# Performance work log

Measured on AMD Instinct MI355X. Metric: run time of the kernel, lower is better.

## Reference

```python
import jax, jax.numpy as jnp
import numpy as np

B, H, W = 64, 512, 512
T = 100           # num_thresholds
R = 8             # defect regions per image (max label id)
BLOCK = 128       # defect regions are 128x128 blocks on a 4x4 grid
SAT = 1.0         # saturation_threshold (relative)


def setup_inputs() -> dict:
    key = jax.random.key(0)
    k1, _ = jax.random.split(key)
    preds = jax.random.uniform(k1, (B, H, W), dtype=jnp.float32)
    thresholds = jnp.linspace(0.0, 1.0, T).astype(jnp.float32)
    # Build a labeled GT mask: R disjoint 128x128 block regions per image,
    # labels 1..R (0 = background). This plays the role of measure.label(target).
    rng = np.random.default_rng(0)
    labels = np.zeros((B, H, W), dtype=np.int32)
    gb = H // BLOCK           # 4 blocks per side -> 16 candidate blocks
    nblocks = gb * gb
    for b in range(B):
        chosen = rng.permutation(nblocks)[:R]
        for rid, blk in enumerate(chosen, start=1):
            r, c = divmod(int(blk), gb)
            labels[b, r * BLOCK:(r + 1) * BLOCK, c * BLOCK:(c + 1) * BLOCK] = rid
    return {"preds": preds, "thresholds": thresholds, "labels": jnp.asarray(labels)}


def reference(preds, thresholds, labels):
    # preds: (B,H,W) float32 in [0,1); thresholds: (T,) sorted; labels: (B,H,W) int32, 0=bg.
    Bn, Hn, Wn = preds.shape
    Tn = thresholds.shape[0]
    flat_s = preds.reshape(-1)
    flat_l = labels.reshape(-1)
    # bucket[p] = number of thresholds <= score[p]; pixel passes thr[t] iff bucket > t.
    bucket = jnp.searchsorted(thresholds, flat_s, side='right')  # int in [0, T]
    # ---- background FP / TN per threshold (exact counts via histogram) ----
    bg = (flat_l == 0).astype(jnp.int32)
    bg_hist = jax.ops.segment_sum(bg, bucket, num_segments=Tn + 1)  # (T+1,)
    bg_total = bg_hist.sum()
    fp = (bg_total - jnp.cumsum(bg_hist)[:Tn]).astype(jnp.float32)  # fp[t] = #bg with score>=thr[t]
    tn = bg_total.astype(jnp.float32) - fp
    # ---- per-region TP per threshold (segmented histogram) ----
    bidx = jnp.repeat(jnp.arange(Bn), Hn * Wn)
    seg = bidx * R + (flat_l - 1)              # region id in [0, B*R)
    comb = seg * (Tn + 1) + bucket
    NSEG = Bn * R * (Tn + 1)
    comb = jnp.where(flat_l > 0, comb, NSEG)   # dump bg pixels in overflow slot
    hist = jax.ops.segment_sum(jnp.ones_like(bucket, dtype=jnp.int32), comb,
                               num_segments=NSEG + 1)[:NSEG].reshape(Bn, R, Tn + 1)
    area = hist.sum(-1)                                       # (B,R) defect areas
    tp = (area[..., None] - jnp.cumsum(hist, -1)[..., :Tn]).astype(jnp.float32)  # (B,R,T)
    sat = jnp.maximum(area.astype(jnp.float32) * SAT, 1.0)    # relative saturation
    valid = (area > 0).astype(jnp.float32)                    # guard empty regions
    spro = jnp.minimum(tp / sat[..., None], 1.0) * valid[..., None]
    spro_sum = spro.sum((0, 1))                               # (T,)
    n_def = jnp.maximum(valid.sum(), 1.0)
    mean_spro = spro_sum / n_def
    # ---- AUC over FPR (max_fpr = 1.0) ----
    denom = fp + tn
    fpr = jnp.where(denom > 0, fp / jnp.maximum(denom, 1.0), 0.0)
    order = jnp.argsort(fpr)
    x = fpr[order]
    y = mean_spro[order]
    auc = jnp.sum((x[1:] - x[:-1]) * (y[1:] + y[:-1]) * 0.5)  # trapezoid rule
    return auc
```

## Files before the change

### kernel.cpp

```cpp
#include <hip/hip_runtime.h>

#define B_N 64
#define H_N 512
#define W_N 512
#define T_N 100
#define TB  101
#define R_N 8
#define NLAB 9
#define BLOCKS_PER_IMG 16
#define PIX_PER_IMG (H_N * W_N)
#define PIX_PER_BLOCK (PIX_PER_IMG / BLOCKS_PER_IMG)

__global__ __launch_bounds__(256) void hist_kernel(
    const float* __restrict__ preds, const int* __restrict__ labels,
    const float* __restrict__ thr,
    int* __restrict__ region_hist,
    int* __restrict__ bg_hist)
{
    __shared__ float s_thr[T_N];
    __shared__ int whist[4][NLAB * TB];

    const int tid  = threadIdx.x;
    const int wave = tid >> 6;

    for (int i = tid; i < 4 * NLAB * TB; i += 256) ((int*)whist)[i] = 0;
    if (tid < T_N) s_thr[tid] = thr[tid];
    __syncthreads();

    const int img   = blockIdx.x / BLOCKS_PER_IMG;
    const int chunk = blockIdx.x % BLOCKS_PER_IMG;
    const long base = (long)img * PIX_PER_IMG + (long)chunk * PIX_PER_BLOCK;
    const float4* p4 = (const float4*)(preds + base);
    const int4*   l4 = (const int4*)(labels + base);
    int* __restrict__ myh = whist[wave];

    const int iters = PIX_PER_BLOCK / (256 * 4);
    for (int it = 0; it < iters; ++it) {
        float4 pv = p4[it * 256 + tid];
        int4   lv = l4[it * 256 + tid];
        float ps[4] = {pv.x, pv.y, pv.z, pv.w};
        int   ls[4] = {lv.x, lv.y, lv.z, lv.w};
#pragma unroll
        for (int j = 0; j < 4; ++j) {
            float s = ps[j];
            int k = (int)(s * (float)(T_N - 1)) + 1;
            k = max(0, min(T_N, k));
            while (k < T_N && s_thr[k] <= s) ++k;
            while (k > 0 && s_thr[k - 1] > s) --k;
            atomicAdd(&myh[ls[j] * TB + k], 1);
        }
    }
    __syncthreads();

    for (int i = tid; i < NLAB * TB; i += 256) {
        int v = whist[0][i] + whist[1][i] + whist[2][i] + whist[3][i];
        if (v) {
            int lab = i / TB;
            int t   = i - lab * TB;
            if (lab == 0)
                atomicAdd(&bg_hist[img * TB + t], v);
            else
                atomicAdd(&region_hist[(img * R_N + (lab - 1)) * TB + t], v);
        }
    }
}

__global__ __launch_bounds__(128) void region_kernel(
    const int* __restrict__ region_hist,
    float* __restrict__ spro_sum,
    int* __restrict__ n_def)
{
    __shared__ float spro_sh[R_N][T_N];
    __shared__ int validc[R_N];
    const int img = blockIdx.x;
    const int tid = threadIdx.x;

    if (tid < R_N) {
        const int* h = &region_hist[(img * R_N + tid) * TB];
        int area = 0;
        for (int t = 0; t < TB; ++t) area += h[t];
        float sat   = fmaxf((float)area, 1.0f);
        float valid = (area > 0) ? 1.0f : 0.0f;
        int csum = 0;
        for (int t = 0; t < T_N; ++t) {
            csum += h[t];
            float tp = (float)(area - csum);
            spro_sh[tid][t] = fminf(tp / sat, 1.0f) * valid;
        }
        validc[tid] = (area > 0) ? 1 : 0;
    }
    __syncthreads();

    if (tid < T_N) {
        float s = 0.0f;
        for (int r = 0; r < R_N; ++r) s += spro_sh[r][tid];
        atomicAdd(&spro_sum[tid], s);
    }
    if (tid == 0) {
        int v = 0;
        for (int r = 0; r < R_N; ++r) v += validc[r];
        atomicAdd(n_def, v);
    }
}

__global__ __launch_bounds__(128) void final_kernel(
    const int* __restrict__ bg_hist,
    const float* __restrict__ spro_sum,
    const int* __restrict__ n_def,
    float* __restrict__ out)
{
    __shared__ int    bgh[TB];
    __shared__ float  fpr_sh[T_N];
    __shared__ float  ms_sh[T_N];
    __shared__ int    order[T_N];
    __shared__ double contrib[T_N];
    const int tid = threadIdx.x;

    if (tid < TB) {
        int s = 0;
        for (int b = 0; b < B_N; ++b) s += bg_hist[b * TB + tid];
        bgh[tid] = s;
    }
    __syncthreads();

    if (tid < T_N) {
        int fp_i = 0;
        for (int k = tid + 1; k < TB; ++k) fp_i += bgh[k];
        int tot = fp_i;
        for (int k = 0; k <= tid; ++k) tot += bgh[k];
        float bgt = (float)tot;
        float fp  = (float)fp_i;
        fpr_sh[tid] = (bgt > 0.0f) ? fp / fmaxf(bgt, 1.0f) : 0.0f;
        float nd = fmaxf((float)(*n_def), 1.0f);
        ms_sh[tid] = spro_sum[tid] / nd;
    }
    __syncthreads();

    if (tid < T_N) {
        float v = fpr_sh[tid];
        int r = 0;
        for (int j = 0; j < T_N; ++j) {
            float u = fpr_sh[j];
            r += (u < v) | ((u == v) & (j < tid));
        }
        order[r] = tid;
    }
    __syncthreads();

    if (tid < T_N - 1) {
        int o0 = order[tid], o1 = order[tid + 1];
        double x0 = fpr_sh[o0], x1 = fpr_sh[o1];
        double y0 = ms_sh[o0],  y1 = ms_sh[o1];
        contrib[tid] = (x1 - x0) * (y0 + y1) * 0.5;
    } else if (tid < T_N) {
        contrib[tid] = 0.0;
    }
    __syncthreads();

    if (tid == 0) {
        double s = 0.0;
        for (int i = 0; i < T_N - 1; ++i) s += contrib[i];
        out[0] = (float)s;
    }
}

extern "C" void kernel_launch(void* const* d_in, const int* in_sizes, int n_in,
                              void* d_out, int out_size, void* d_ws, size_t ws_size,
                              hipStream_t stream) {
    const float* preds  = (const float*)d_in[0];
    const float* thr    = (const float*)d_in[1];
    const int*   labels = (const int*)d_in[2];
    float* out = (float*)d_out;

    int*   region_hist = (int*)d_ws;
    int*   bg_hist     = region_hist + B_N * R_N * TB;
    float* spro_sum    = (float*)(bg_hist + B_N * TB);
    int*   n_def       = (int*)(spro_sum + T_N);

    size_t zbytes = sizeof(int) * (size_t)(B_N * R_N * TB + B_N * TB)
                  + sizeof(float) * T_N + sizeof(int);
    hipMemsetAsync(d_ws, 0, zbytes, stream);

    hist_kernel<<<B_N * BLOCKS_PER_IMG, 256, 0, stream>>>(preds, labels, thr,
                                                          region_hist, bg_hist);
    region_kernel<<<B_N, 128, 0, stream>>>(region_hist, spro_sum, n_def);
    final_kernel<<<1, 128, 0, stream>>>(bg_hist, spro_sum, n_def, out);
}
```

Baseline: 166.9 us.

## Split histogram across more blocks and parallelize region/final reductions via shared memory

Doubles the number of histogram blocks per image so more workgroups run concurrently across the GPU's CUs. The region kernel stages each image's histograms in shared memory and computes per-threshold TP suffix sums with one thread per threshold, replacing the serial per-region loop run by only 8 threads. The final kernel stages the background histograms in LDS with a cooperative load before reducing them. The cost is more redundant summation per thread and more global atomics from the histogram flush.

```diff
diff --git a/kernel.cpp b/kernel.cpp
--- a/kernel.cpp
+++ b/kernel.cpp
@@ -7,7 +7,7 @@
 #define TB  101
 #define R_N 8
 #define NLAB 9
-#define BLOCKS_PER_IMG 16
+#define BLOCKS_PER_IMG 32
 #define PIX_PER_IMG (H_N * W_N)
 #define PIX_PER_BLOCK (PIX_PER_IMG / BLOCKS_PER_IMG)
 
@@ -65,50 +65,54 @@
     }
 }
 
-__global__ __launch_bounds__(128) void region_kernel(
+__global__ __launch_bounds__(256) void region_kernel(
     const int* __restrict__ region_hist,
     float* __restrict__ spro_sum,
     int* __restrict__ n_def)
 {
-    __shared__ float spro_sh[R_N][T_N];
-    __shared__ int validc[R_N];
+    __shared__ int   h_sh[R_N * TB];
+    __shared__ float area_sh[R_N];
     const int img = blockIdx.x;
     const int tid = threadIdx.x;
 
+    for (int i = tid; i < R_N * TB; i += 256)
+        h_sh[i] = region_hist[img * (R_N * TB) + i];
+    __syncthreads();
+
     if (tid < R_N) {
-        const int* h = &region_hist[(img * R_N + tid) * TB];
-        int area = 0;
-        for (int t = 0; t < TB; ++t) area += h[t];
-        float sat   = fmaxf((float)area, 1.0f);
-        float valid = (area > 0) ? 1.0f : 0.0f;
-        int csum = 0;
-        for (int t = 0; t < T_N; ++t) {
-            csum += h[t];
-            float tp = (float)(area - csum);
-            spro_sh[tid][t] = fminf(tp / sat, 1.0f) * valid;
-        }
-        validc[tid] = (area > 0) ? 1 : 0;
+        int a = 0;
+        for (int t = 0; t < TB; ++t) a += h_sh[tid * TB + t];
+        area_sh[tid] = (float)a;
     }
     __syncthreads();
 
     if (tid < T_N) {
         float s = 0.0f;
-        for (int r = 0; r < R_N; ++r) s += spro_sh[r][tid];
+#pragma unroll
+        for (int r = 0; r < R_N; ++r) {
+            int tp = 0;
+            for (int k = tid + 1; k < TB; ++k) tp += h_sh[r * TB + k];
+            float area  = area_sh[r];
+            float sat   = fmaxf(area, 1.0f);
+            float valid = (area > 0.0f) ? 1.0f : 0.0f;
+            s += fminf((float)tp / sat, 1.0f) * valid;
+        }
         atomicAdd(&spro_sum[tid], s);
     }
     if (tid == 0) {
         int v = 0;
-        for (int r = 0; r < R_N; ++r) v += validc[r];
+        for (int r = 0; r < R_N; ++r) v += (area_sh[r] > 0.0f) ? 1 : 0;
         atomicAdd(n_def, v);
     }
 }
 
-__global__ __launch_bounds__(128) void final_kernel(
+__global__ __launch_bounds__(256) void final_kernel(
     const int* __restrict__ bg_hist,
     const float* __restrict__ spro_sum,
     const int* __restrict__ n_def,
     float* __restrict__ out)
 {
+    __shared__ int    stage[B_N * TB];
     __shared__ int    bgh[TB];
     __shared__ float  fpr_sh[T_N];
     __shared__ float  ms_sh[T_N];
@@ -116,9 +120,12 @@
     __shared__ double contrib[T_N];
     const int tid = threadIdx.x;
 
+    for (int i = tid; i < B_N * TB; i += 256) stage[i] = bg_hist[i];
+    __syncthreads();
+
     if (tid < TB) {
         int s = 0;
-        for (int b = 0; b < B_N; ++b) s += bg_hist[b * TB + tid];
+        for (int b = 0; b < B_N; ++b) s += stage[b * TB + tid];
         bgh[tid] = s;
     }
     __syncthreads();
@@ -183,6 +190,6 @@
 
     hist_kernel<<<B_N * BLOCKS_PER_IMG, 256, 0, stream>>>(preds, labels, thr,
                                                           region_hist, bg_hist);
-    region_kernel<<<B_N, 128, 0, stream>>>(region_hist, spro_sum, n_def);
-    final_kernel<<<1, 128, 0, stream>>>(bg_hist, spro_sum, n_def, out);
+    region_kernel<<<B_N, 256, 0, stream>>>(region_hist, spro_sum, n_def);
+    final_kernel<<<1, 256, 0, stream>>>(bg_hist, spro_sum, n_def, out);
 }
```

Result: slower. 171.8 us (+2.9%).
